# Optimization experiments

Measured on AMD Instinct MI355X. Metric: run time of the kernel, lower is better.

The kernel has to match this reference:

```python
import jax, jax.numpy as jnp
import numpy as np

LEAK = 0.2
N, C, T, H, DOUT = 512, 16, 15, 32, 32


def setup_inputs() -> dict:
    key = jax.random.key(0)
    k = jax.random.split(key, 5)
    x = jax.random.normal(k[0], (N, C), dtype=jnp.float32)
    adj = jax.random.uniform(k[1], (N, N, T), dtype=jnp.float32)
    W1 = jax.random.normal(k[2], (2 * C, T + 1, H), dtype=jnp.float32) * 0.05
    W2 = jax.random.normal(k[3], (2 * C, T + 1, DOUT), dtype=jnp.float32) * 0.05
    W3 = jax.random.normal(k[4], (C, H), dtype=jnp.float32) * 0.05
    return {"x": x, "adj": adj, "W1": W1, "W2": W2, "W3": W3}


def reference(x, adj, W1, W2, W3):
    n, c = x.shape
    # input_diag: [N,N,C,1], diagonal copy of node features
    diag = jnp.einsum('mn,ni->mni', jnp.eye(n, dtype=x.dtype), x)[..., None]
    # D = concat(adj-weighted broadcast of x, diag) along edge-type axis -> [N,N,C,T+1]
    D = jnp.concatenate([jnp.einsum('mnt,ni->mnit', adj, x), diag], axis=3)
    # symmetrize along channel axis -> [N,N,2C,T+1]
    D = jnp.concatenate([D, jnp.transpose(D, (1, 0, 2, 3))], axis=2)
    K = jnp.einsum('mnit,ith->mnh', D, W1)   # [N,N,H]
    V = jnp.einsum('mnit,itd->mnd', D, W2)   # [N,N,DOUT]
    Q = x @ W3                               # [N,H]
    logits1 = jnp.einsum('nh,nmh->nm', Q, K)
    logits2 = jnp.einsum('mh,nmh->nm', Q, K)
    s1 = jax.nn.softmax(logits1, axis=1)
    s2 = jax.nn.softmax(logits2, axis=0)
    temp = jnp.einsum('nm,nmd->nd', s1, V) + jnp.einsum('nm,nmd->md', s2, V)
    return jnp.maximum(temp, LEAK * temp)  # lrelu
```

## Files before the change

### kernel.cpp

```cpp
#include <hip/hip_runtime.h>
#include <hip/hip_bf16.h>

#define NNODE 512
#define CCH   16
#define TT    15
#define TP    16
#define HH    32
#define DD    32

typedef unsigned short u16;
typedef unsigned int   u32;
typedef short bf8 __attribute__((ext_vector_type(8)));
typedef float f4  __attribute__((ext_vector_type(4)));

__device__ __forceinline__ float bf2f(u16 v) {
    union { u32 u; float f; } x; x.u = ((u32)v) << 16; return x.f;
}
__device__ __forceinline__ u16 f2bf(float f) {
    union { float f; u32 u; } x; x.f = f;
    u32 u = x.u;
    return (u16)((u + 0x7FFFu + ((u >> 16) & 1u)) >> 16);
}
__device__ __forceinline__ void unpack8(uint4 p, float* o) {
    o[0]=bf2f((u16)(p.x & 0xffffu)); o[1]=bf2f((u16)(p.x >> 16));
    o[2]=bf2f((u16)(p.y & 0xffffu)); o[3]=bf2f((u16)(p.y >> 16));
    o[4]=bf2f((u16)(p.z & 0xffffu)); o[5]=bf2f((u16)(p.z >> 16));
    o[6]=bf2f((u16)(p.w & 0xffffu)); o[7]=bf2f((u16)(p.w >> 16));
}
__device__ __forceinline__ uint4 pack8(const u16* v) {
    return make_uint4((u32)v[0]|((u32)v[1]<<16), (u32)v[2]|((u32)v[3]<<16),
                      (u32)v[4]|((u32)v[5]<<16), (u32)v[6]|((u32)v[7]<<16));
}

__global__ __launch_bounds__(256) void k_prep_adjp(
    const float* __restrict__ x, const float* __restrict__ W1,
    const float* __restrict__ W2, const float* __restrict__ W3,
    const float* __restrict__ adj,
    u16* __restrict__ A1, u16* __restrict__ B1,
    u16* __restrict__ A2T, u16* __restrict__ B2T,
    u16* __restrict__ Qb, float* __restrict__ QAd, float* __restrict__ QB,
    u16* __restrict__ adjP, u16* __restrict__ adjPT)
{
    int tid = threadIdx.x;
    if (blockIdx.x < 512) {
        int n = blockIdx.x;
        __shared__ alignas(16) float xs[CCH];
        __shared__ alignas(16) float A1row[512], B1row[512];
        __shared__ alignas(16) float A2row[512], B2row[512];
        __shared__ alignas(16) float Qs[HH];
        if (tid < CCH) xs[tid] = x[n*CCH + tid];
        __syncthreads();
        float xr[CCH];
        #pragma unroll
        for (int i=0;i<CCH;i++) xr[i]=xs[i];
        #pragma unroll
        for (int rep=0; rep<2; rep++) {
            int c = tid + rep*256;
            float a1=0.f,b1=0.f,a2=0.f,b2=0.f;
            #pragma unroll
            for (int i=0;i<CCH;i++) {
                a1 += xr[i]*W1[i*512 + c];
                b1 += xr[i]*W1[(CCH+i)*512 + c];
                a2 += xr[i]*W2[i*512 + c];
                b2 += xr[i]*W2[(CCH+i)*512 + c];
            }
            A1[(size_t)n*512 + c]=f2bf(a1); B1[(size_t)n*512 + c]=f2bf(b1);
            A1row[c]=a1; B1row[c]=b1; A2row[c]=a2; B2row[c]=b2;
        }
        if (tid < HH) {
            float q=0.f;
            #pragma unroll
            for (int i=0;i<CCH;i++) q += xr[i]*W3[i*HH + tid];
            Qs[tid]=q; Qb[(size_t)n*HH + tid]=f2bf(q);
        }
        __syncthreads();
        if (tid < TP) {
            float qa=0.f, qb=0.f;
            #pragma unroll
            for (int h=0;h<HH;h++) { qa += Qs[h]*A1row[tid*HH+h]; qb += Qs[h]*B1row[tid*HH+h]; }
            QAd[(size_t)n*TP + tid]=qa; QB[(size_t)n*TP + tid]=qb;
        }
        {
            int d = tid >> 3, t0 = (tid & 7) * 2;
            u32 pa = (u32)f2bf(A2row[t0*32 + d]) | ((u32)f2bf(A2row[(t0+1)*32 + d]) << 16);
            u32 pb = (u32)f2bf(B2row[t0*32 + d]) | ((u32)f2bf(B2row[(t0+1)*32 + d]) << 16);
            *(u32*)(A2T + (size_t)d*8192 + n*16 + t0) = pa;
            *(u32*)(B2T + (size_t)d*8192 + n*16 + t0) = pb;
        }
    } else {
        int b = blockIdx.x - 512;
        int n0 = (b >> 4) * 32, m0 = (b & 15) * 32;
        __shared__ alignas(16) u16 s[32*520];
        #pragma unroll
        for (int i = 0; i < 60; i++) {
            int e = tid + i*256;
            int nl = e / 480; int rem = e - nl*480;
            int ml = rem / 15; int t = rem - ml*15;
            float v = adj[((size_t)(n0+nl)*512 + (m0+ml))*TT + t];
            s[nl*520 + ml*16 + t] = f2bf(v);
        }
        #pragma unroll
        for (int i = 0; i < 4; i++) {
            int e = tid + i*256; int nl = e >> 5, ml = e & 31;
            s[nl*520 + ml*16 + 15] = ((n0+nl) == (m0+ml)) ? (u16)0x3F80 : (u16)0;
        }
        __syncthreads();
        #pragma unroll
        for (int i = 0; i < 8; i++) {
            int c = tid + i*256;
            int nl = c >> 6, off = (c & 63) * 8;
            uint4 vv = *(const uint4*)(s + nl*520 + off);
            *(uint4*)(adjP + (size_t)(n0+nl)*8192 + m0*16 + off) = vv;
        }
        #pragma unroll
        for (int i = 0; i < 8; i++) {
            int c = tid + i*256;
            int ml = c >> 6, nlh = c & 63, nl = nlh >> 1, half = nlh & 1;
            uint4 vv = *(const uint4*)(s + nl*520 + ml*16 + half*8);
            *(uint4*)(adjPT + (size_t)(m0+ml)*8192 + (n0+nl)*16 + half*8) = vv;
        }
    }
}

__global__ __launch_bounds__(256) void k_logits(
    const u16* __restrict__ Qb, const u16* __restrict__ A1, const u16* __restrict__ B1,
    const u16* __restrict__ adjP, const u16* __restrict__ adjPT,
    const float* __restrict__ QAd, const float* __restrict__ QB,
    float* __restrict__ L1, float* __restrict__ L2T)
{
    const int m0 = blockIdx.x * 16, n0 = blockIdx.y * 16;
    const int tid = threadIdx.x;
    const int wv = tid >> 6, lane = tid & 63, l15 = lane & 15, quad = lane >> 4;
    __shared__ alignas(16) float sL1[16*17];
    __shared__ alignas(16) float sL2[16*17];

    bf8 qbN = *(const bf8*)(Qb + (size_t)(n0 + l15)*32 + quad*8);
    bf8 qbM = *(const bf8*)(Qb + (size_t)(m0 + l15)*32 + quad*8);
    float4 qb4 = *(const float4*)(QB  + (size_t)(n0 + l15)*TP + quad*4);
    float4 qa4 = *(const float4*)(QAd + (size_t)(m0 + l15)*TP + quad*4);

    #pragma unroll
    for (int j = 0; j < 4; j++) {
        int m = m0 + wv*4 + j;
        bf8 aA1 = *(const bf8*)(A1 + (size_t)m*512 + l15*32 + quad*8);
        f4 z = {0.f,0.f,0.f,0.f};
        f4 g = __builtin_amdgcn_mfma_f32_16x16x32_bf16(aA1, qbN, z, 0, 0, 0);
        uint2 ax = *(const uint2*)(adjPT + (size_t)m*8192 + (n0 + l15)*16 + quad*4);
        uint2 ay = *(const uint2*)(adjP  + (size_t)m*8192 + (n0 + l15)*16 + quad*4);
        float v;
        v = bf2f((u16)(ax.x & 0xffffu)) * g[0];
        v = fmaf(bf2f((u16)(ax.x >> 16)),     g[1], v);
        v = fmaf(bf2f((u16)(ax.y & 0xffffu)), g[2], v);
        v = fmaf(bf2f((u16)(ax.y >> 16)),     g[3], v);
        v = fmaf(bf2f((u16)(ay.x & 0xffffu)), qb4.x, v);
        v = fmaf(bf2f((u16)(ay.x >> 16)),     qb4.y, v);
        v = fmaf(bf2f((u16)(ay.y & 0xffffu)), qb4.z, v);
        v = fmaf(bf2f((u16)(ay.y >> 16)),     qb4.w, v);
        v += __shfl_xor(v, 16, 64);
        v += __shfl_xor(v, 32, 64);
        if (quad == 0) sL1[l15*17 + wv*4 + j] = v;
    }
    #pragma unroll
    for (int j = 0; j < 4; j++) {
        int n = n0 + wv*4 + j;
        bf8 aB1 = *(const bf8*)(B1 + (size_t)n*512 + l15*32 + quad*8);
        f4 z = {0.f,0.f,0.f,0.f};
        f4 h = __builtin_amdgcn_mfma_f32_16x16x32_bf16(aB1, qbM, z, 0, 0, 0);
        uint2 ax = *(const uint2*)(adjPT + (size_t)n*8192 + (m0 + l15)*16 + quad*4);
        uint2 ay = *(const uint2*)(adjP  + (size_t)n*8192 + (m0 + l15)*16 + quad*4);
        float v;
        v = bf2f((u16)(ax.x & 0xffffu)) * h[0];
        v = fmaf(bf2f((u16)(ax.x >> 16)),     h[1], v);
        v = fmaf(bf2f((u16)(ax.y & 0xffffu)), h[2], v);
        v = fmaf(bf2f((u16)(ax.y >> 16)),     h[3], v);
        v = fmaf(bf2f((u16)(ay.x & 0xffffu)), qa4.x, v);
        v = fmaf(bf2f((u16)(ay.x >> 16)),     qa4.y, v);
        v = fmaf(bf2f((u16)(ay.y & 0xffffu)), qa4.z, v);
        v = fmaf(bf2f((u16)(ay.y >> 16)),     qa4.w, v);
        v += __shfl_xor(v, 16, 64);
        v += __shfl_xor(v, 32, 64);
        if (quad == 0) sL2[l15*17 + wv*4 + j] = v;
    }
    __syncthreads();
    int row = tid >> 4, col = tid & 15;
    L1 [(size_t)(n0+row)*NNODE + m0 + col] = sL1[row*17+col];
    L2T[(size_t)(m0+row)*NNODE + n0 + col] = sL2[row*17+col];
}

__global__ __launch_bounds__(256) void k_stats(
    const float* __restrict__ L1, const float* __restrict__ L2T,
    float2* __restrict__ stats, float* __restrict__ temp,
    float* __restrict__ u1, float* __restrict__ v2)
{
    int tid = threadIdx.x;
    int g0 = blockIdx.x * 256 + tid;
    if (g0 < 16384) temp[g0] = 0.f;
    else if (g0 < 24576) u1[g0 - 16384] = 0.f;
    else if (g0 < 32768) v2[g0 - 24576] = 0.f;

    int wv = tid >> 6, lane = tid & 63;
    int g = blockIdx.x * 4 + wv;
    const float* rw = (g < NNODE) ? (L1 + (size_t)g*NNODE)
                                  : (L2T + (size_t)(g - NNODE)*NNODE);
    float4 a = *(const float4*)(rw + lane*8);
    float4 b = *(const float4*)(rw + lane*8 + 4);
    float mx = fmaxf(fmaxf(fmaxf(a.x,a.y),fmaxf(a.z,a.w)),
                     fmaxf(fmaxf(b.x,b.y),fmaxf(b.z,b.w)));
    #pragma unroll
    for (int o=32; o; o>>=1) mx = fmaxf(mx, __shfl_xor(mx, o, 64));
    float sm = __expf(a.x-mx)+__expf(a.y-mx)+__expf(a.z-mx)+__expf(a.w-mx)
             + __expf(b.x-mx)+__expf(b.y-mx)+__expf(b.z-mx)+__expf(b.w-mx);
    #pragma unroll
    for (int o=32; o; o>>=1) sm += __shfl_xor(sm, o, 64);
    if (lane == 0) { float2 st; st.x = mx; st.y = 1.0f/sm; stats[g] = st; }
}

__global__ __launch_bounds__(256) void k_smx_gemm(
    const float* __restrict__ L1, const float* __restrict__ L2T,
    const u16* __restrict__ adjP, const u16* __restrict__ adjPT,
    const u16* __restrict__ A2T, const u16* __restrict__ B2T,
    const float2* __restrict__ stats,
    float* __restrict__ temp, float* __restrict__ u1, float* __restrict__ v2)
{
    const int j0 = blockIdx.x * 16, kc = blockIdx.y, dir = blockIdx.z;
    const int tid = threadIdx.x;
    const int wv = tid >> 6, lane = tid & 63, l15 = lane & 15, quad = lane >> 4;
    const float* Lbase = dir ? L2T : L1;

    __shared__ alignas(16) u16 Wt[16*256];
    __shared__ alignas(16) float redb[4][512];
    __shared__ float2 sst[16];

    if (tid < 16) sst[tid] = stats[dir*NNODE + j0 + tid];
    __syncthreads();

    {
        int j = tid >> 4, cb = tid & 15;
        int m = kc*16 + cb;
        float2 st = sst[j];
        float s0 = __expf(Lbase[(size_t)(j0+j)*NNODE + m] - st.x) * st.y;

        const uint4* pp = (const uint4*)(adjP + (size_t)(j0+j)*8192 + m*16);
        float av[16]; unpack8(pp[0], av); unpack8(pp[1], av+8);
        u16 wo[16];
        #pragma unroll
        for (int e=0;e<16;e++) wo[e] = f2bf(s0*av[e]);
        #pragma unroll
        for (int q=0;q<2;q++) {
            int sl = (cb*2 + q) ^ (j & 7);
            *(uint4*)&Wt[j*256 + sl*8] = pack8(wo + q*8);
        }

        const uint4* qq = (const uint4*)(adjPT + (size_t)(j0+j)*8192 + m*16);
        float tv[16]; unpack8(qq[0], tv); unpack8(qq[1], tv+8);
        float ut[16];
        #pragma unroll
        for (int t=0;t<16;t++) ut[t] = s0*tv[t];
        #pragma unroll
        for (int i=0;i<8;i++) {
            float v0 = (lane&1) ? ut[i] : ut[i+8];
            float r0 = __shfl_xor(v0, 1, 64);
            ut[i] = ((lane&1) ? ut[i+8] : ut[i]) + r0;
        }
        #pragma unroll
        for (int i=0;i<4;i++) {
            float v0 = (lane&2) ? ut[i] : ut[i+4];
            float r0 = __shfl_xor(v0, 2, 64);
            ut[i] = ((lane&2) ? ut[i+4] : ut[i]) + r0;
        }
        #pragma unroll
        for (int i=0;i<2;i++) {
            float v0 = (lane&4) ? ut[i] : ut[i+2];
            float r0 = __shfl_xor(v0, 4, 64);
            ut[i] = ((lane&4) ? ut[i+2] : ut[i]) + r0;
        }
        {
            float v0 = (lane&8) ? ut[0] : ut[1];
            float r0 = __shfl_xor(v0, 8, 64);
            ut[0] = ((lane&8) ? ut[1] : ut[0]) + r0;
        }
        int tm = ((cb&1)<<3) | ((cb&2)<<1) | ((cb&4)>>1) | ((cb&8)>>3);
        atomicAdd((dir ? v2 : u1) + (size_t)(j0+j)*TP + tm, ut[0]);
    }
    __syncthreads();

    {
        const u16* Bmat = dir ? B2T : A2T;
        f4 acc0 = {0.f,0.f,0.f,0.f}, acc1 = {0.f,0.f,0.f,0.f};
        #pragma unroll
        for (int st2 = 0; st2 < 2; st2++) {
            int s = wv*2 + st2;
            bf8 afr = *(const bf8*)&Wt[l15*256 + (((s*4 + quad) ^ (l15 & 7)) << 3)];
            bf8 b0 = *(const bf8*)(Bmat + (size_t)(l15)*8192    + kc*256 + s*32 + quad*8);
            bf8 b1 = *(const bf8*)(Bmat + (size_t)(16+l15)*8192 + kc*256 + s*32 + quad*8);
            acc0 = __builtin_amdgcn_mfma_f32_16x16x32_bf16(afr, b0, acc0, 0, 0, 0);
            acc1 = __builtin_amdgcn_mfma_f32_16x16x32_bf16(afr, b1, acc1, 0, 0, 0);
        }
        #pragma unroll
        for (int r = 0; r < 4; r++) {
            redb[wv][      (quad*4+r)*16 + l15] = acc0[r];
            redb[wv][256 + (quad*4+r)*16 + l15] = acc1[r];
        }
    }
    __syncthreads();
    #pragma unroll
    for (int h = 0; h < 2; h++) {
        int o = tid + h*256;
        int jj = o >> 5, d = o & 31;
        int idx = (d >> 4)*256 + jj*16 + (d & 15);
        float v = redb[0][idx] + redb[1][idx] + redb[2][idx] + redb[3][idx];
        atomicAdd(&temp[(size_t)(j0 + jj)*DD + d], v);
    }
}

__global__ __launch_bounds__(256) void k_final(
    const float* __restrict__ temp, const float* __restrict__ u1, const float* __restrict__ v2,
    const u16* __restrict__ A2T, const u16* __restrict__ B2T, float* __restrict__ out)
{
    int base = blockIdx.x * 256 + threadIdx.x;
    int j = base >> 5, d = base & 31;
    float acc = temp[(size_t)j*DD + d];
    const uint4* pb2 = (const uint4*)(B2T + (size_t)d*8192 + j*16);
    const uint4* pa2 = (const uint4*)(A2T + (size_t)d*8192 + j*16);
    float bv[16], avv[16];
    unpack8(pb2[0], bv);  unpack8(pb2[1], bv+8);
    unpack8(pa2[0], avv); unpack8(pa2[1], avv+8);
    #pragma unroll
    for (int t = 0; t < 16; t++)
        acc += u1[(size_t)j*TP + t]*bv[t] + v2[(size_t)j*TP + t]*avv[t];
    out[(size_t)j*DD + d] = fmaxf(acc, 0.2f*acc);
}

extern "C" void kernel_launch(void* const* d_in, const int* in_sizes, int n_in,
                              void* d_out, int out_size, void* d_ws, size_t ws_size,
                              hipStream_t stream)
{
    (void)in_sizes; (void)n_in; (void)out_size; (void)ws_size;
    const float* x   = (const float*)d_in[0];
    const float* adj = (const float*)d_in[1];
    const float* W1  = (const float*)d_in[2];
    const float* W2  = (const float*)d_in[3];
    const float* W3  = (const float*)d_in[4];

    char* ws = (char*)d_ws;
    u16*   adjP  = (u16*)(ws);
    u16*   adjPT = (u16*)(ws + 0x800000);
    u16*   A1    = (u16*)(ws + 0x1000000);
    u16*   B1    = (u16*)(ws + 0x1080000);
    u16*   A2T   = (u16*)(ws + 0x1100000);
    u16*   B2T   = (u16*)(ws + 0x1180000);
    u16*   Qb    = (u16*)(ws + 0x1200000);
    float* QAd   = (float*)(ws + 0x1210000);
    float* QB    = (float*)(ws + 0x1220000);
    float* L1    = (float*)(ws + 0x1300000);
    float* L2T   = (float*)(ws + 0x1400000);
    float* temp  = (float*)(ws + 0x1500000);
    float* u1    = (float*)(ws + 0x1510000);
    float* v2    = (float*)(ws + 0x1520000);
    float2* stats= (float2*)(ws + 0x1530000);

    k_prep_adjp<<<768, 256, 0, stream>>>(x, W1, W2, W3, adj,
                                         A1, B1, A2T, B2T, Qb, QAd, QB, adjP, adjPT);
    k_logits<<<dim3(32,32), 256, 0, stream>>>(Qb, A1, B1, adjP, adjPT, QAd, QB, L1, L2T);
    k_stats<<<256, 256, 0, stream>>>(L1, L2T, stats, temp, u1, v2);
    k_smx_gemm<<<dim3(32,32,2), 256, 0, stream>>>(L1, L2T, adjP, adjPT, A2T, B2T,
                                                  stats, temp, u1, v2);
    k_final<<<64, 256, 0, stream>>>(temp, u1, v2, A2T, B2T, (float*)d_out);
}
```

Baseline: 103.2 us.

## Fold softmax stats and final epilogue into producer kernels via last-block counters

Removes the separate stats and final kernels. The last logits block to finish each row or column stripe, detected with atomic counters, computes the softmax max and sum for those rows. The last softmax-GEMM block per j-tile applies the epilogue and LeakyReLU. Zeroing of the accumulators and counters moves into extra blocks of the prep kernel. This saves two launches but adds fences, atomics and a serialized tail on the last-arriving blocks.

After: 335.8 us. 3.26x slower.

```diff
diff --git a/kernel.cpp b/kernel.cpp
--- a/kernel.cpp
+++ b/kernel.cpp
@@ -39,9 +39,19 @@
     u16* __restrict__ A1, u16* __restrict__ B1,
     u16* __restrict__ A2T, u16* __restrict__ B2T,
     u16* __restrict__ Qb, float* __restrict__ QAd, float* __restrict__ QB,
-    u16* __restrict__ adjP, u16* __restrict__ adjPT)
+    u16* __restrict__ adjP, u16* __restrict__ adjPT,
+    float* __restrict__ temp, float* __restrict__ u1, float* __restrict__ v2,
+    u32* __restrict__ ctrs)
 {
     int tid = threadIdx.x;
+    if (blockIdx.x >= 768) {
+        int idx = (blockIdx.x - 768) * 256 + tid;
+        if (idx < 16384) temp[idx] = 0.f;
+        else if (idx < 24576) u1[idx - 16384] = 0.f;
+        else if (idx < 32768) v2[idx - 24576] = 0.f;
+        else if (idx < 32864) ctrs[idx - 32768] = 0u;
+        return;
+    }
     if (blockIdx.x < 512) {
         int n = blockIdx.x;
         __shared__ alignas(16) float xs[CCH];
@@ -126,7 +136,8 @@
     const u16* __restrict__ Qb, const u16* __restrict__ A1, const u16* __restrict__ B1,
     const u16* __restrict__ adjP, const u16* __restrict__ adjPT,
     const float* __restrict__ QAd, const float* __restrict__ QB,
-    float* __restrict__ L1, float* __restrict__ L2T)
+    float* __restrict__ L1, float* __restrict__ L2T,
+    float2* __restrict__ stats, u32* __restrict__ ctrN, u32* __restrict__ ctrM)
 {
     const int m0 = blockIdx.x * 16, n0 = blockIdx.y * 16;
     const int tid = threadIdx.x;
@@ -185,34 +196,52 @@
     int row = tid >> 4, col = tid & 15;
     L1 [(size_t)(n0+row)*NNODE + m0 + col] = sL1[row*17+col];
     L2T[(size_t)(m0+row)*NNODE + n0 + col] = sL2[row*17+col];
-}
-
-__global__ __launch_bounds__(256) void k_stats(
-    const float* __restrict__ L1, const float* __restrict__ L2T,
-    float2* __restrict__ stats, float* __restrict__ temp,
-    float* __restrict__ u1, float* __restrict__ v2)
-{
-    int tid = threadIdx.x;
-    int g0 = blockIdx.x * 256 + tid;
-    if (g0 < 16384) temp[g0] = 0.f;
-    else if (g0 < 24576) u1[g0 - 16384] = 0.f;
-    else if (g0 < 32768) v2[g0 - 24576] = 0.f;
-
-    int wv = tid >> 6, lane = tid & 63;
-    int g = blockIdx.x * 4 + wv;
-    const float* rw = (g < NNODE) ? (L1 + (size_t)g*NNODE)
-                                  : (L2T + (size_t)(g - NNODE)*NNODE);
-    float4 a = *(const float4*)(rw + lane*8);
-    float4 b = *(const float4*)(rw + lane*8 + 4);
-    float mx = fmaxf(fmaxf(fmaxf(a.x,a.y),fmaxf(a.z,a.w)),
-                     fmaxf(fmaxf(b.x,b.y),fmaxf(b.z,b.w)));
-    #pragma unroll
-    for (int o=32; o; o>>=1) mx = fmaxf(mx, __shfl_xor(mx, o, 64));
-    float sm = __expf(a.x-mx)+__expf(a.y-mx)+__expf(a.z-mx)+__expf(a.w-mx)
-             + __expf(b.x-mx)+__expf(b.y-mx)+__expf(b.z-mx)+__expf(b.w-mx);
-    #pragma unroll
-    for (int o=32; o; o>>=1) sm += __shfl_xor(sm, o, 64);
-    if (lane == 0) { float2 st; st.x = mx; st.y = 1.0f/sm; stats[g] = st; }
+
+    __threadfence();
+    __shared__ int doN, doM;
+    if (tid == 0) {
+        doN = (atomicAdd(&ctrN[blockIdx.y], 1u) == 31u) ? 1 : 0;
+        doM = (atomicAdd(&ctrM[blockIdx.x], 1u) == 31u) ? 1 : 0;
+    }
+    __syncthreads();
+    if (doN) {
+        __threadfence();
+        #pragma unroll
+        for (int rr = 0; rr < 4; rr++) {
+            int r = n0 + wv*4 + rr;
+            const float* rw = L1 + (size_t)r*NNODE;
+            float4 a = *(const float4*)(rw + lane*8);
+            float4 b = *(const float4*)(rw + lane*8 + 4);
+            float mx = fmaxf(fmaxf(fmaxf(a.x,a.y),fmaxf(a.z,a.w)),
+                             fmaxf(fmaxf(b.x,b.y),fmaxf(b.z,b.w)));
+            #pragma unroll
+            for (int o=32; o; o>>=1) mx = fmaxf(mx, __shfl_xor(mx, o, 64));
+            float sm = __expf(a.x-mx)+__expf(a.y-mx)+__expf(a.z-mx)+__expf(a.w-mx)
+                     + __expf(b.x-mx)+__expf(b.y-mx)+__expf(b.z-mx)+__expf(b.w-mx);
+            #pragma unroll
+            for (int o=32; o; o>>=1) sm += __shfl_xor(sm, o, 64);
+            if (lane == 0) { float2 st; st.x = mx; st.y = 1.0f/sm; stats[r] = st; }
+        }
+    }
+    if (doM) {
+        __threadfence();
+        #pragma unroll
+        for (int rr = 0; rr < 4; rr++) {
+            int r = m0 + wv*4 + rr;
+            const float* rw = L2T + (size_t)r*NNODE;
+            float4 a = *(const float4*)(rw + lane*8);
+            float4 b = *(const float4*)(rw + lane*8 + 4);
+            float mx = fmaxf(fmaxf(fmaxf(a.x,a.y),fmaxf(a.z,a.w)),
+                             fmaxf(fmaxf(b.x,b.y),fmaxf(b.z,b.w)));
+            #pragma unroll
+            for (int o=32; o; o>>=1) mx = fmaxf(mx, __shfl_xor(mx, o, 64));
+            float sm = __expf(a.x-mx)+__expf(a.y-mx)+__expf(a.z-mx)+__expf(a.w-mx)
+                     + __expf(b.x-mx)+__expf(b.y-mx)+__expf(b.z-mx)+__expf(b.w-mx);
+            #pragma unroll
+            for (int o=32; o; o>>=1) sm += __shfl_xor(sm, o, 64);
+            if (lane == 0) { float2 st; st.x = mx; st.y = 1.0f/sm; stats[NNODE + r] = st; }
+        }
+    }
 }
 
 __global__ __launch_bounds__(256) void k_smx_gemm(
@@ -220,7 +249,8 @@
     const u16* __restrict__ adjP, const u16* __restrict__ adjPT,
     const u16* __restrict__ A2T, const u16* __restrict__ B2T,
     const float2* __restrict__ stats,
-    float* __restrict__ temp, float* __restrict__ u1, float* __restrict__ v2)
+    float* __restrict__ temp, float* __restrict__ u1, float* __restrict__ v2,
+    u32* __restrict__ ctrJ, float* __restrict__ out)
 {
     const int j0 = blockIdx.x * 16, kc = blockIdx.y, dir = blockIdx.z;
     const int tid = threadIdx.x;
@@ -311,24 +341,34 @@
         float v = redb[0][idx] + redb[1][idx] + redb[2][idx] + redb[3][idx];
         atomicAdd(&temp[(size_t)(j0 + jj)*DD + d], v);
     }
-}
-
-__global__ __launch_bounds__(256) void k_final(
-    const float* __restrict__ temp, const float* __restrict__ u1, const float* __restrict__ v2,
-    const u16* __restrict__ A2T, const u16* __restrict__ B2T, float* __restrict__ out)
-{
-    int base = blockIdx.x * 256 + threadIdx.x;
-    int j = base >> 5, d = base & 31;
-    float acc = temp[(size_t)j*DD + d];
-    const uint4* pb2 = (const uint4*)(B2T + (size_t)d*8192 + j*16);
-    const uint4* pa2 = (const uint4*)(A2T + (size_t)d*8192 + j*16);
-    float bv[16], avv[16];
-    unpack8(pb2[0], bv);  unpack8(pb2[1], bv+8);
-    unpack8(pa2[0], avv); unpack8(pa2[1], avv+8);
-    #pragma unroll
-    for (int t = 0; t < 16; t++)
-        acc += u1[(size_t)j*TP + t]*bv[t] + v2[(size_t)j*TP + t]*avv[t];
-    out[(size_t)j*DD + d] = fmaxf(acc, 0.2f*acc);
+
+    __threadfence();
+    __shared__ int doF;
+    if (tid == 0) doF = (atomicAdd(&ctrJ[blockIdx.x], 1u) == 63u) ? 1 : 0;
+    __syncthreads();
+    if (doF) {
+        __threadfence();
+        __shared__ float uL[256], vL[256];
+        uL[tid] = atomicAdd(&u1[(size_t)j0*TP + tid], 0.0f);
+        vL[tid] = atomicAdd(&v2[(size_t)j0*TP + tid], 0.0f);
+        __syncthreads();
+        #pragma unroll
+        for (int h = 0; h < 2; h++) {
+            int o = tid + h*256;
+            int jj = o >> 5, d = o & 31;
+            int j = j0 + jj;
+            float acc = atomicAdd(&temp[(size_t)j*DD + d], 0.0f);
+            const uint4* pb2 = (const uint4*)(B2T + (size_t)d*8192 + j*16);
+            const uint4* pa2 = (const uint4*)(A2T + (size_t)d*8192 + j*16);
+            float bv[16], avv[16];
+            unpack8(pb2[0], bv);  unpack8(pb2[1], bv+8);
+            unpack8(pa2[0], avv); unpack8(pa2[1], avv+8);
+            #pragma unroll
+            for (int t = 0; t < 16; t++)
+                acc += uL[jj*16+t]*bv[t] + vL[jj*16+t]*avv[t];
+            out[(size_t)j*DD + d] = fmaxf(acc, 0.2f*acc);
+        }
+    }
 }
 
 extern "C" void kernel_launch(void* const* d_in, const int* in_sizes, int n_in,
@@ -358,12 +398,17 @@
     float* u1    = (float*)(ws + 0x1510000);
     float* v2    = (float*)(ws + 0x1520000);
     float2* stats= (float2*)(ws + 0x1530000);
-
-    k_prep_adjp<<<768, 256, 0, stream>>>(x, W1, W2, W3, adj,
-                                         A1, B1, A2T, B2T, Qb, QAd, QB, adjP, adjPT);
-    k_logits<<<dim3(32,32), 256, 0, stream>>>(Qb, A1, B1, adjP, adjPT, QAd, QB, L1, L2T);
-    k_stats<<<256, 256, 0, stream>>>(L1, L2T, stats, temp, u1, v2);
+    u32*   ctrs  = (u32*)  (ws + 0x1540000);
+    u32*   ctrN  = ctrs;
+    u32*   ctrM  = ctrs + 32;
+    u32*   ctrJ  = ctrs + 64;
+
+    k_prep_adjp<<<897, 256, 0, stream>>>(x, W1, W2, W3, adj,
+                                         A1, B1, A2T, B2T, Qb, QAd, QB, adjP, adjPT,
+                                         temp, u1, v2, ctrs);
+    k_logits<<<dim3(32,32), 256, 0, stream>>>(Qb, A1, B1, adjP, adjPT, QAd, QB,
+                                              L1, L2T, stats, ctrN, ctrM);
     k_smx_gemm<<<dim3(32,32,2), 256, 0, stream>>>(L1, L2T, adjP, adjPT, A2T, B2T,
-                                                  stats, temp, u1, v2);
-    k_final<<<64, 256, 0, stream>>>(temp, u1, v2, A2T, B2T, (float*)d_out);
-}
+                                                  stats, temp, u1, v2, ctrJ,
+                                                  (float*)d_out);
+}
```

## Fuse softmax stats into logits kernel and drop separate stats launch

Applied to the files above, without the earlier changes.

Removes the k_stats kernel. Each k_logits block now computes per-tile partial max and sum-of-exp for its 16x16 tile and writes them to a partial-stats buffer. k_smx_gemm merges the 32 partials per row with an online-softmax reduction. Zeroing of the accumulators moves into extra blocks of the prep kernel. This saves one launch and a re-read of the logits, at the cost of more shuffles in logits and redundant partial merges in every smx_gemm block.

After: 102.2 us. Within noise of the previous version (-0.9%).

```diff
diff --git a/kernel.cpp b/kernel.cpp
--- a/kernel.cpp
+++ b/kernel.cpp
@@ -39,9 +39,17 @@
     u16* __restrict__ A1, u16* __restrict__ B1,
     u16* __restrict__ A2T, u16* __restrict__ B2T,
     u16* __restrict__ Qb, float* __restrict__ QAd, float* __restrict__ QB,
-    u16* __restrict__ adjP, u16* __restrict__ adjPT)
+    u16* __restrict__ adjP, u16* __restrict__ adjPT,
+    float* __restrict__ temp, float* __restrict__ u1, float* __restrict__ v2)
 {
     int tid = threadIdx.x;
+    if (blockIdx.x >= 768) {
+        int idx = (blockIdx.x - 768) * 256 + tid;
+        if (idx < 16384) temp[idx] = 0.f;
+        else if (idx < 24576) u1[idx - 16384] = 0.f;
+        else if (idx < 32768) v2[idx - 24576] = 0.f;
+        return;
+    }
     if (blockIdx.x < 512) {
         int n = blockIdx.x;
         __shared__ alignas(16) float xs[CCH];
@@ -126,7 +134,8 @@
     const u16* __restrict__ Qb, const u16* __restrict__ A1, const u16* __restrict__ B1,
     const u16* __restrict__ adjP, const u16* __restrict__ adjPT,
     const float* __restrict__ QAd, const float* __restrict__ QB,
-    float* __restrict__ L1, float* __restrict__ L2T)
+    float* __restrict__ L1, float* __restrict__ L2T,
+    float2* __restrict__ statsP)
 {
     const int m0 = blockIdx.x * 16, n0 = blockIdx.y * 16;
     const int tid = threadIdx.x;
@@ -183,43 +192,36 @@
     }
     __syncthreads();
     int row = tid >> 4, col = tid & 15;
-    L1 [(size_t)(n0+row)*NNODE + m0 + col] = sL1[row*17+col];
-    L2T[(size_t)(m0+row)*NNODE + n0 + col] = sL2[row*17+col];
-}
-
-__global__ __launch_bounds__(256) void k_stats(
-    const float* __restrict__ L1, const float* __restrict__ L2T,
-    float2* __restrict__ stats, float* __restrict__ temp,
-    float* __restrict__ u1, float* __restrict__ v2)
-{
-    int tid = threadIdx.x;
-    int g0 = blockIdx.x * 256 + tid;
-    if (g0 < 16384) temp[g0] = 0.f;
-    else if (g0 < 24576) u1[g0 - 16384] = 0.f;
-    else if (g0 < 32768) v2[g0 - 24576] = 0.f;
-
-    int wv = tid >> 6, lane = tid & 63;
-    int g = blockIdx.x * 4 + wv;
-    const float* rw = (g < NNODE) ? (L1 + (size_t)g*NNODE)
-                                  : (L2T + (size_t)(g - NNODE)*NNODE);
-    float4 a = *(const float4*)(rw + lane*8);
-    float4 b = *(const float4*)(rw + lane*8 + 4);
-    float mx = fmaxf(fmaxf(fmaxf(a.x,a.y),fmaxf(a.z,a.w)),
-                     fmaxf(fmaxf(b.x,b.y),fmaxf(b.z,b.w)));
-    #pragma unroll
-    for (int o=32; o; o>>=1) mx = fmaxf(mx, __shfl_xor(mx, o, 64));
-    float sm = __expf(a.x-mx)+__expf(a.y-mx)+__expf(a.z-mx)+__expf(a.w-mx)
-             + __expf(b.x-mx)+__expf(b.y-mx)+__expf(b.z-mx)+__expf(b.w-mx);
-    #pragma unroll
-    for (int o=32; o; o>>=1) sm += __shfl_xor(sm, o, 64);
-    if (lane == 0) { float2 st; st.x = mx; st.y = 1.0f/sm; stats[g] = st; }
+    float v1 = sL1[row*17+col];
+    float v2v = sL2[row*17+col];
+    L1 [(size_t)(n0+row)*NNODE + m0 + col] = v1;
+    L2T[(size_t)(m0+row)*NNODE + n0 + col] = v2v;
+
+    float mx1 = v1, mx2 = v2v;
+    #pragma unroll
+    for (int o=1; o<16; o<<=1) {
+        mx1 = fmaxf(mx1, __shfl_xor(mx1, o, 64));
+        mx2 = fmaxf(mx2, __shfl_xor(mx2, o, 64));
+    }
+    float s1 = __expf(v1 - mx1), s2 = __expf(v2v - mx2);
+    #pragma unroll
+    for (int o=1; o<16; o<<=1) {
+        s1 += __shfl_xor(s1, o, 64);
+        s2 += __shfl_xor(s2, o, 64);
+    }
+    if (col == 0) {
+        float2 st1; st1.x = mx1; st1.y = s1;
+        float2 st2; st2.x = mx2; st2.y = s2;
+        statsP[(size_t)(n0+row)*32 + blockIdx.x]         = st1;
+        statsP[(size_t)(NNODE + m0+row)*32 + blockIdx.y] = st2;
+    }
 }
 
 __global__ __launch_bounds__(256) void k_smx_gemm(
     const float* __restrict__ L1, const float* __restrict__ L2T,
     const u16* __restrict__ adjP, const u16* __restrict__ adjPT,
     const u16* __restrict__ A2T, const u16* __restrict__ B2T,
-    const float2* __restrict__ stats,
+    const float2* __restrict__ statsP,
     float* __restrict__ temp, float* __restrict__ u1, float* __restrict__ v2)
 {
     const int j0 = blockIdx.x * 16, kc = blockIdx.y, dir = blockIdx.z;
@@ -231,7 +233,21 @@
     __shared__ alignas(16) float redb[4][512];
     __shared__ float2 sst[16];
 
-    if (tid < 16) sst[tid] = stats[dir*NNODE + j0 + tid];
+    {
+        int j = tid >> 4, pp = tid & 15;
+        const float2* sp = statsP + (size_t)(dir*NNODE + j0 + j)*32;
+        float2 a = sp[pp*2], b = sp[pp*2+1];
+        float mx = fmaxf(a.x, b.x);
+        float sm = a.y*__expf(a.x - mx) + b.y*__expf(b.x - mx);
+        #pragma unroll
+        for (int o=1; o<16; o<<=1) {
+            float omx = __shfl_xor(mx, o, 64), osm = __shfl_xor(sm, o, 64);
+            float nmx = fmaxf(mx, omx);
+            sm = sm*__expf(mx - nmx) + osm*__expf(omx - nmx);
+            mx = nmx;
+        }
+        if (pp == 0) { float2 st; st.x = mx; st.y = 1.0f/sm; sst[j] = st; }
+    }
     __syncthreads();
 
     {
@@ -357,13 +373,14 @@
     float* temp  = (float*)(ws + 0x1500000);
     float* u1    = (float*)(ws + 0x1510000);
     float* v2    = (float*)(ws + 0x1520000);
-    float2* stats= (float2*)(ws + 0x1530000);
-
-    k_prep_adjp<<<768, 256, 0, stream>>>(x, W1, W2, W3, adj,
-                                         A1, B1, A2T, B2T, Qb, QAd, QB, adjP, adjPT);
-    k_logits<<<dim3(32,32), 256, 0, stream>>>(Qb, A1, B1, adjP, adjPT, QAd, QB, L1, L2T);
-    k_stats<<<256, 256, 0, stream>>>(L1, L2T, stats, temp, u1, v2);
+    float2* statsP=(float2*)(ws + 0x1530000);
+
+    k_prep_adjp<<<896, 256, 0, stream>>>(x, W1, W2, W3, adj,
+                                         A1, B1, A2T, B2T, Qb, QAd, QB, adjP, adjPT,
+                                         temp, u1, v2);
+    k_logits<<<dim3(32,32), 256, 0, stream>>>(Qb, A1, B1, adjP, adjPT, QAd, QB,
+                                              L1, L2T, statsP);
     k_smx_gemm<<<dim3(32,32,2), 256, 0, stream>>>(L1, L2T, adjP, adjPT, A2T, B2T,
-                                                  stats, temp, u1, v2);
+                                                  statsP, temp, u1, v2);
     k_final<<<64, 256, 0, stream>>>(temp, u1, v2, A2T, B2T, (float*)d_out);
 }
```
